# Optimization experiments

Measured on AMD Instinct MI355X. Metric: run time of the kernel, lower is better.

The kernel has to match this reference:

```python
import jax, jax.numpy as jnp
import numpy as np

ETA = 0.1
DT = 1.0
H, DH = 8, 64


def setup_inputs() -> dict:
    key = jax.random.key(0)
    ks = jax.random.split(key, 7)
    B, N, D = 4, 2048, 1024
    s = 0.02
    return {
        "x": jax.random.normal(ks[0], (B, N, D), dtype=jnp.float32),
        "gamma": jax.random.uniform(ks[1], (B, N), dtype=jnp.float32),
        "state": jnp.zeros((B, H, DH, DH), dtype=jnp.float32),
        "Wq": (jax.random.normal(ks[2], (D, H * DH), dtype=jnp.float32) * s),
        "Wk": (jax.random.normal(ks[3], (D, H * DH), dtype=jnp.float32) * s),
        "Wv": (jax.random.normal(ks[4], (D, H * DH), dtype=jnp.float32) * s),
        "Wo": (jax.random.normal(ks[5], (H * DH, D), dtype=jnp.float32) * s),
        "bo": jnp.zeros((D,), dtype=jnp.float32),
    }


def reference(x, gamma, state, Wq, Wk, Wv, Wo, bo):
    B, N, D = x.shape
    # projections -> (N, B, H, DH) for scan over time
    q = (x @ Wq).reshape(B, N, H, DH).transpose(1, 0, 2, 3)
    k = (x @ Wk).reshape(B, N, H, DH).transpose(1, 0, 2, 3)
    v = (x @ Wv).reshape(B, N, H, DH).transpose(1, 0, 2, 3)
    # decay = exp(-clamp(gamma*dt, max=10)) -> (N, B)
    decay = jnp.exp(-jnp.minimum(gamma * DT, 10.0)).T

    def step(st, inp):
        q_t, k_t, v_t, d_t = inp  # (B,H,DH),(B,H,DH),(B,H,DH),(B,)
        # W_new = exp(-Gamma*dt) * stop_grad(W_old) + eta * k^T v
        st_new = d_t[:, None, None, None] * jax.lax.stop_gradient(st) \
                 + ETA * jnp.einsum('bhi,bhj->bhij', k_t, v_t)
        y_t = jnp.einsum('bhij,bhj->bhi', st_new, q_t)  # (B,H,DH)
        return st_new, y_t

    state_final, ys = jax.lax.scan(step, state, (q, k, v, decay))
    # ys: (N, B, H, DH) -> (B, N, H*DH)
    y = ys.transpose(1, 0, 2, 3).reshape(B, N, H * DH)
    out = y @ Wo + bo
    return out, state_final
```

## Files before the change

kernel.cpp:

```cpp
#include <hip/hip_runtime.h>

#define ETA 0.1f
#define BATCH 4
#define SEQ 2048
#define DMODEL 1024
#define NH 8
#define DHEAD 64
#define HD 512
#define QKVW 1536
#define CH 64
#define NCH (SEQ / CH)

typedef float f32x4 __attribute__((ext_vector_type(4)));
typedef short short8 __attribute__((ext_vector_type(8)));
typedef short short4v __attribute__((ext_vector_type(4)));

static __device__ __forceinline__ ushort f2bf(float f) {
  union { float f; unsigned u; } x; x.f = f;
  unsigned r = (x.u + 0x7fffu + ((x.u >> 16) & 1u)) >> 16;
  return (ushort)r;
}
static __device__ __forceinline__ float bf2f(ushort u) {
  union { unsigned u; float f; } x; x.u = ((unsigned)u) << 16;
  return x.f;
}

#define GLDS16(g, l)                                                    \
  __builtin_amdgcn_global_load_lds(                                     \
      (const __attribute__((address_space(1))) unsigned int*)(const void*)(g), \
      (__attribute__((address_space(3))) unsigned int*)(void*)(l), 16, 0, 0)

__global__ __launch_bounds__(256) void convx_kernel(
    const float* __restrict__ x, ushort* __restrict__ xb) {
  size_t i = ((size_t)blockIdx.x * 256 + threadIdx.x) * 16;
  ushort t[16];
#pragma unroll
  for (int u = 0; u < 4; ++u) {
    f32x4 v = *(const f32x4*)&x[i + u * 4];
#pragma unroll
    for (int e = 0; e < 4; ++e) t[u * 4 + e] = f2bf(v[e]);
  }
  *(short8*)&xb[i] = *(short8*)&t[0];
  *(short8*)&xb[i + 8] = *(short8*)&t[8];
}

__global__ __launch_bounds__(256) void convw_kernel(
    const float* __restrict__ Wq, const float* __restrict__ Wk,
    const float* __restrict__ Wv, const float* __restrict__ Wo,
    ushort* __restrict__ Wt, ushort* __restrict__ Wot) {
  const int m = blockIdx.y;
  const int bx = blockIdx.x;
  const int tid = threadIdx.x;
  __shared__ float T[32][33];

  const float* src;
  ushort* dst;
  int srcN, dstK, k0, n0, rowOff;
  if (m < 3) {
    src = (m == 0) ? Wq : ((m == 1) ? Wk : Wv);
    srcN = 512; dstK = 1024;
    k0 = (bx >> 4) << 5; n0 = (bx & 15) << 5;
    dst = Wt; rowOff = m * 512;
  } else {
    src = Wo; srcN = 1024; dstK = 512;
    k0 = (bx >> 5) << 5; n0 = (bx & 31) << 5;
    dst = Wot; rowOff = 0;
  }
  const int r = tid >> 3, c4 = (tid & 7) << 2;
  f32x4 v = *(const f32x4*)&src[(size_t)(k0 + r) * srcN + n0 + c4];
  T[r][c4 + 0] = v[0]; T[r][c4 + 1] = v[1];
  T[r][c4 + 2] = v[2]; T[r][c4 + 3] = v[3];
  __syncthreads();
  short4v o;
#pragma unroll
  for (int e = 0; e < 4; ++e) o[e] = (short)f2bf(T[c4 + e][r]);
  *(short4v*)&dst[(size_t)(rowOff + n0 + r) * dstK + k0 + c4] = o;
}

template <bool OUT_BF16>
__global__ __launch_bounds__(512, 4) void gemm_bt_kernel(
    const ushort* __restrict__ A, const ushort* __restrict__ Bt,
    void* __restrict__ Cv, const float* __restrict__ bias,
    int M, int N, int K) {
  const int tiles_n = N >> 8;
  const int nwg = gridDim.x;
  const int bid = blockIdx.x;
  const int swz = (bid & 7) * (nwg >> 3) + (bid >> 3);
  const int bm = swz / tiles_n;
  const int bn = swz % tiles_n;
  const int tid = threadIdx.x;
  const int w = tid >> 6, lane = tid & 63;
  const int wr = w >> 2, wc = w & 3;
  const int fr = lane & 15, fq = lane >> 4;

  __shared__ ushort As[2][128][32];
  __shared__ ushort Bs[2][256][32];

  f32x4 acc[4][4];
#pragma unroll
  for (int mi = 0; mi < 4; ++mi)
#pragma unroll
    for (int ni = 0; ni < 4; ++ni) acc[mi][ni] = f32x4{0.f, 0.f, 0.f, 0.f};

  const int sr = tid >> 2;
  const int sc = (tid & 3) << 3;
  const ushort* ga  = A  + (size_t)(bm * 128 + sr) * K + sc;
  const ushort* gb0 = Bt + (size_t)(bn * 256 + sr) * K + sc;
  const ushort* gb1 = Bt + (size_t)(bn * 256 + 128 + sr) * K + sc;

  const int nt = K >> 5;

  {
    ushort* la = &As[0][0][0] + (size_t)tid * 8;
    ushort* lb = &Bs[0][0][0] + (size_t)tid * 8;
    GLDS16(ga, la);
    GLDS16(gb0, lb);
    GLDS16(gb1, lb + 4096);
  }
  asm volatile("s_waitcnt vmcnt(0)" ::: "memory");
  __syncthreads();

  for (int t = 0; t < nt; ++t) {
    if (t + 1 < nt) {
      const int nb = (t + 1) & 1;
      const int kt = (t + 1) << 5;
      ushort* la = &As[nb][0][0] + (size_t)tid * 8;
      ushort* lb = &Bs[nb][0][0] + (size_t)tid * 8;
      GLDS16(ga + kt, la);
      GLDS16(gb0 + kt, lb);
      GLDS16(gb1 + kt, lb + 4096);
    }
    const int cb = t & 1;
    short8 a[4], b[4];
#pragma unroll
    for (int mi = 0; mi < 4; ++mi)
      a[mi] = *(const short8*)&As[cb][wr * 64 + mi * 16 + fr][fq * 8];
#pragma unroll
    for (int ni = 0; ni < 4; ++ni)
      b[ni] = *(const short8*)&Bs[cb][wc * 64 + ni * 16 + fr][fq * 8];
#pragma unroll
    for (int mi = 0; mi < 4; ++mi)
#pragma unroll
      for (int ni = 0; ni < 4; ++ni)
        acc[mi][ni] = __builtin_amdgcn_mfma_f32_16x16x32_bf16(
            a[mi], b[ni], acc[mi][ni], 0, 0, 0);
    asm volatile("s_waitcnt vmcnt(0)" ::: "memory");
    __syncthreads();
  }

#pragma unroll
  for (int ni = 0; ni < 4; ++ni) {
    const int gc = bn * 256 + wc * 64 + ni * 16 + fr;
    float badd = (!OUT_BF16 && bias) ? bias[gc] : 0.f;
#pragma unroll
    for (int mi = 0; mi < 4; ++mi) {
#pragma unroll
      for (int r = 0; r < 4; ++r) {
        const int gr = bm * 128 + wr * 64 + mi * 16 + fq * 4 + r;
        if (OUT_BF16) {
          ((ushort*)Cv)[(size_t)gr * N + gc] = f2bf(acc[mi][ni][r]);
        } else {
          ((float*)Cv)[(size_t)gr * N + gc] = acc[mi][ni][r] + badd;
        }
      }
    }
  }
}

__global__ __launch_bounds__(256) void intra_kernel(
    const ushort* __restrict__ qkv, const float* __restrict__ gamma,
    ushort* __restrict__ ybf, ushort* __restrict__ S, float* __restrict__ clb) {
  const int bx = blockIdx.x;
  const int c = bx & (NCH - 1);
  const int h = (bx >> 5) & (NH - 1);
  const int b = bx >> 8;
  const int tid = threadIdx.x;
  const int w = tid >> 6, lane = tid & 63;
  const int fr = lane & 15, fq = lane >> 4;

  __shared__ ushort Qs[64][72];
  __shared__ ushort Vs[64][72];
  __shared__ ushort KT[64][72];
  __shared__ ushort VT[64][72];
  __shared__ ushort Ps[64][72];
  __shared__ float cumS[64];
  __shared__ float clS;

  const int p = tid >> 2, d0 = (tid & 3) * 16;
  const ushort* base = &qkv[((size_t)b * SEQ + c * CH + p) * QKVW + h * 64 + d0];
  short8 q0 = *(const short8*)base;
  short8 q1 = *(const short8*)(base + 8);
  short8 k0 = *(const short8*)(base + 512);
  short8 k1 = *(const short8*)(base + 520);
  short8 v0 = *(const short8*)(base + 1024);
  short8 v1 = *(const short8*)(base + 1032);

  if (tid < 64) {
    float g = gamma[(size_t)b * SEQ + c * CH + tid];
    float prod = expf(-fminf(g, 10.f));
#pragma unroll
    for (int off = 1; off < 64; off <<= 1) {
      float o = __shfl_up(prod, off);
      if (tid >= off) prod *= o;
    }
    cumS[tid] = prod;
    if (tid == 63) clS = prod;
  }
  __syncthreads();

  {
    const float cp = cumS[p];
    const float rc = 1.f / cp;
    ushort tq[16], tv[16];
#pragma unroll
    for (int j = 0; j < 8; ++j) {
      tq[j]     = f2bf(bf2f((ushort)q0[j]) * cp);
      tq[8 + j] = f2bf(bf2f((ushort)q1[j]) * cp);
      tv[j]     = f2bf(bf2f((ushort)v0[j]) * rc);
      tv[8 + j] = f2bf(bf2f((ushort)v1[j]) * rc);
      KT[d0 + j][p] = (ushort)k0[j];
      KT[d0 + 8 + j][p] = (ushort)k1[j];
      VT[d0 + j][p] = tv[j];
      VT[d0 + 8 + j][p] = tv[8 + j];
    }
    *(short8*)&Qs[p][d0] = *(short8*)&tq[0];
    *(short8*)&Qs[p][d0 + 8] = *(short8*)&tq[8];
    *(short8*)&Vs[p][d0] = *(short8*)&tv[0];
    *(short8*)&Vs[p][d0 + 8] = *(short8*)&tv[8];
  }
  __syncthreads();

  const int arow = w * 16 + fr;
  {
    short8 a0 = *(const short8*)&Qs[arow][fq * 8];
    short8 a1 = *(const short8*)&Qs[arow][32 + fq * 8];
#pragma unroll
    for (int cf = 0; cf < 4; ++cf) {
      f32x4 acc = {0.f, 0.f, 0.f, 0.f};
      if (cf <= w) {
        short8 b0 = *(const short8*)&Vs[cf * 16 + fr][fq * 8];
        short8 b1 = *(const short8*)&Vs[cf * 16 + fr][32 + fq * 8];
        acc = __builtin_amdgcn_mfma_f32_16x16x32_bf16(a0, b0, acc, 0, 0, 0);
        acc = __builtin_amdgcn_mfma_f32_16x16x32_bf16(a1, b1, acc, 0, 0, 0);
      }
#pragma unroll
      for (int r = 0; r < 4; ++r) {
        int pi = w * 16 + fq * 4 + r, si = cf * 16 + fr;
        Ps[pi][si] = f2bf((si <= pi) ? acc[r] * ETA : 0.f);
      }
    }
  }
  __syncthreads();

  {
    short8 p0 = *(const short8*)&Ps[arow][fq * 8];
    short8 p1 = *(const short8*)&Ps[arow][32 + fq * 8];
    short8 ka0 = *(const short8*)&KT[arow][fq * 8];
    short8 ka1 = *(const short8*)&KT[arow][32 + fq * 8];
    const float scl = ETA * clS;
    const size_t yrow0 = (size_t)b * SEQ + c * CH;
    ushort* Sp = &S[(((size_t)(b * NH + h)) * NCH + c) << 12];
#pragma unroll
    for (int cf = 0; cf < 4; ++cf) {
      short8 bk0 = *(const short8*)&KT[cf * 16 + fr][fq * 8];
      short8 bk1 = *(const short8*)&KT[cf * 16 + fr][32 + fq * 8];
      f32x4 accY = {0.f, 0.f, 0.f, 0.f};
      accY = __builtin_amdgcn_mfma_f32_16x16x32_bf16(p0, bk0, accY, 0, 0, 0);
      accY = __builtin_amdgcn_mfma_f32_16x16x32_bf16(p1, bk1, accY, 0, 0, 0);
      short8 bv0 = *(const short8*)&VT[cf * 16 + fr][fq * 8];
      short8 bv1 = *(const short8*)&VT[cf * 16 + fr][32 + fq * 8];
      f32x4 accS = {0.f, 0.f, 0.f, 0.f};
      accS = __builtin_amdgcn_mfma_f32_16x16x32_bf16(ka0, bv0, accS, 0, 0, 0);
      accS = __builtin_amdgcn_mfma_f32_16x16x32_bf16(ka1, bv1, accS, 0, 0, 0);
#pragma unroll
      for (int r = 0; r < 4; ++r) {
        int row = w * 16 + fq * 4 + r;
        int col = cf * 16 + fr;
        ybf[(yrow0 + row) * HD + h * 64 + col] = f2bf(accY[r]);
        Sp[row * 64 + col] = f2bf(accS[r] * scl);
      }
    }
  }
  if (tid == 0 && h == 0) clb[b * NCH + c] = clS;
}

__global__ __launch_bounds__(256) void prop_kernel(
    const float* __restrict__ state0, const ushort* __restrict__ S,
    const float* __restrict__ clb, ushort* __restrict__ stash,
    float* __restrict__ state_out) {
  const int bh = blockIdx.x >> 2, rg = blockIdx.x & 3;
  const int b = bh >> 3;
  const int tid = threadIdx.x;
  const int i = rg * 16 + (tid >> 4);
  const int j0 = (tid & 15) * 4;
  const size_t off = ((size_t)bh * 64 + i) * 64 + j0;
  const size_t coff = (size_t)i * 64 + j0;

  f32x4 st = *(const f32x4*)&state0[off];
#pragma unroll 4
  for (int c = 0; c < NCH; ++c) {
    const size_t base = (((size_t)bh * NCH + c) << 12) + coff;
    short4v sv;
#pragma unroll
    for (int e = 0; e < 4; ++e) sv[e] = (short)f2bf(st[e]);
    *(short4v*)&stash[base] = sv;
    short4v s = *(const short4v*)&S[base];
    float clv = clb[b * NCH + c];
#pragma unroll
    for (int e = 0; e < 4; ++e) st[e] = st[e] * clv + bf2f((ushort)s[e]);
  }
  *(f32x4*)&state_out[off] = st;
}

__global__ __launch_bounds__(256) void inter_kernel(
    const ushort* __restrict__ qkv, const float* __restrict__ gamma,
    const ushort* __restrict__ stash, ushort* __restrict__ ybf) {
  const int bx = blockIdx.x;
  const int c = bx & (NCH - 1);
  const int h = (bx >> 5) & (NH - 1);
  const int b = bx >> 8;
  const int tid = threadIdx.x;
  const int w = tid >> 6, lane = tid & 63;
  const int fr = lane & 15, fq = lane >> 4;

  __shared__ ushort Qs[64][72];
  __shared__ ushort Bs[64][72];
  __shared__ float cumS[64];

  const int p = tid >> 2, d0 = (tid & 3) * 16;
  const ushort* qp = &qkv[((size_t)b * SEQ + c * CH + p) * QKVW + h * 64 + d0];
  short8 q0 = *(const short8*)qp;
  short8 q1 = *(const short8*)(qp + 8);
  const size_t sb = ((((size_t)(b * NH + h)) * NCH + c) << 12) + (size_t)p * 64 + d0;
  short8 s0 = *(const short8*)&stash[sb];
  short8 s1 = *(const short8*)&stash[sb + 8];

  if (tid < 64) {
    float g = gamma[(size_t)b * SEQ + c * CH + tid];
    float prod = expf(-fminf(g, 10.f));
#pragma unroll
    for (int off = 1; off < 64; off <<= 1) {
      float o = __shfl_up(prod, off);
      if (tid >= off) prod *= o;
    }
    cumS[tid] = prod;
  }
  __syncthreads();

  {
    const float cp = cumS[p];
    ushort tq[16];
#pragma unroll
    for (int j = 0; j < 8; ++j) {
      tq[j]     = f2bf(bf2f((ushort)q0[j]) * cp);
      tq[8 + j] = f2bf(bf2f((ushort)q1[j]) * cp);
    }
    *(short8*)&Qs[p][d0] = *(short8*)&tq[0];
    *(short8*)&Qs[p][d0 + 8] = *(short8*)&tq[8];
    *(short8*)&Bs[p][d0] = s0;
    *(short8*)&Bs[p][d0 + 8] = s1;
  }
  __syncthreads();

  const int arow = w * 16 + fr;
  short8 a0 = *(const short8*)&Qs[arow][fq * 8];
  short8 a1 = *(const short8*)&Qs[arow][32 + fq * 8];
  const size_t yrow0 = (size_t)b * SEQ + c * CH;
#pragma unroll
  for (int cf = 0; cf < 4; ++cf) {
    short8 b0 = *(const short8*)&Bs[cf * 16 + fr][fq * 8];
    short8 b1 = *(const short8*)&Bs[cf * 16 + fr][32 + fq * 8];
    f32x4 acc = {0.f, 0.f, 0.f, 0.f};
    acc = __builtin_amdgcn_mfma_f32_16x16x32_bf16(a0, b0, acc, 0, 0, 0);
    acc = __builtin_amdgcn_mfma_f32_16x16x32_bf16(a1, b1, acc, 0, 0, 0);
#pragma unroll
    for (int r = 0; r < 4; ++r) {
      int row = w * 16 + fq * 4 + r;
      int col = cf * 16 + fr;
      size_t idx = (yrow0 + row) * HD + h * 64 + col;
      ybf[idx] = f2bf(bf2f(ybf[idx]) + acc[r]);
    }
  }
}

extern "C" void kernel_launch(void* const* d_in, const int* in_sizes, int n_in,
                              void* d_out, int out_size, void* d_ws, size_t ws_size,
                              hipStream_t stream) {
  const float* x      = (const float*)d_in[0];
  const float* gamma  = (const float*)d_in[1];
  const float* state0 = (const float*)d_in[2];
  const float* Wq     = (const float*)d_in[3];
  const float* Wk     = (const float*)d_in[4];
  const float* Wv     = (const float*)d_in[5];
  const float* Wo     = (const float*)d_in[6];
  const float* bo     = (const float*)d_in[7];

  float* out = (float*)d_out;
  float* state_out = out + (size_t)BATCH * SEQ * DMODEL;

  const int M = BATCH * SEQ;

  ushort* xb  = (ushort*)d_ws;
  ushort* wt  = xb + (size_t)M * DMODEL;
  ushort* wot = wt + (size_t)QKVW * DMODEL;
  ushort* qkv = wot + (size_t)DMODEL * HD;
  ushort* ybf = qkv + (size_t)M * QKVW;
  ushort* Sb  = ybf + (size_t)M * HD;
  ushort* stash = Sb + (size_t)BATCH * NH * NCH * 4096;
  float*  clb   = (float*)(stash + (size_t)BATCH * NH * NCH * 4096);

  dim3 blk(256);
  dim3 blkg(512);

  convx_kernel<<<dim3((M * DMODEL) / (256 * 16)), blk, 0, stream>>>(x, xb);
  convw_kernel<<<dim3(512, 4), blk, 0, stream>>>(Wq, Wk, Wv, Wo, wt, wot);

  gemm_bt_kernel<true><<<dim3((M / 128) * (QKVW / 256)), blkg, 0, stream>>>(
      xb, wt, qkv, nullptr, M, QKVW, DMODEL);

  intra_kernel<<<dim3(BATCH * NH * NCH), blk, 0, stream>>>(
      qkv, gamma, ybf, Sb, clb);
  prop_kernel<<<dim3(BATCH * NH * 4), blk, 0, stream>>>(
      state0, Sb, clb, stash, state_out);
  inter_kernel<<<dim3(BATCH * NH * NCH), blk, 0, stream>>>(
      qkv, gamma, stash, ybf);

  gemm_bt_kernel<false><<<dim3((M / 128) * (DMODEL / 256)), blkg, 0, stream>>>(
      ybf, wot, out, bo, M, DMODEL, HD);
}
```

Measured before the change: 99.15 us.

## Use 128x128 GEMM tiles with triple-buffered LDS prefetch pipeline

The bf16 GEMM moves from 512-thread 128x256 tiles to 256-thread 128x128 tiles, doubling the block count. It replaces the double buffer with a three-stage LDS ring, issuing loads two tiles ahead. Partial vmcnt waits let later loads stay in flight while the current tile computes. The aim is to hide global-load latency and improve SM fill, at the cost of more B-tile reloads and more blocks.

```diff
diff --git a/kernel.cpp b/kernel.cpp
--- a/kernel.cpp
+++ b/kernel.cpp
@@ -78,11 +78,11 @@
 }
 
 template <bool OUT_BF16>
-__global__ __launch_bounds__(512, 4) void gemm_bt_kernel(
+__global__ __launch_bounds__(256, 3) void gemm_bt_kernel(
     const ushort* __restrict__ A, const ushort* __restrict__ Bt,
     void* __restrict__ Cv, const float* __restrict__ bias,
     int M, int N, int K) {
-  const int tiles_n = N >> 8;
+  const int tiles_n = N >> 7;
   const int nwg = gridDim.x;
   const int bid = blockIdx.x;
   const int swz = (bid & 7) * (nwg >> 3) + (bid >> 3);
@@ -90,11 +90,11 @@
   const int bn = swz % tiles_n;
   const int tid = threadIdx.x;
   const int w = tid >> 6, lane = tid & 63;
-  const int wr = w >> 2, wc = w & 3;
+  const int wr = w >> 1, wc = w & 1;
   const int fr = lane & 15, fq = lane >> 4;
 
-  __shared__ ushort As[2][128][32];
-  __shared__ ushort Bs[2][256][32];
+  __shared__ ushort As[3][128][32];
+  __shared__ ushort Bs[3][128][32];
 
   f32x4 acc[4][4];
 #pragma unroll
@@ -102,35 +102,33 @@
 #pragma unroll
     for (int ni = 0; ni < 4; ++ni) acc[mi][ni] = f32x4{0.f, 0.f, 0.f, 0.f};
 
-  const int sr = tid >> 2;
-  const int sc = (tid & 3) << 3;
-  const ushort* ga  = A  + (size_t)(bm * 128 + sr) * K + sc;
-  const ushort* gb0 = Bt + (size_t)(bn * 256 + sr) * K + sc;
-  const ushort* gb1 = Bt + (size_t)(bn * 256 + 128 + sr) * K + sc;
+  const int lw = lane >> 2;
+  const int lc = (lane & 3) << 3;
+  const ushort* ga = A + (size_t)(bm * 128 + w * 32 + lw) * K + lc;
+  const ushort* gb = Bt + (size_t)(bn * 128 + w * 32 + lw) * K + lc;
+  const size_t rstep = (size_t)16 * K;
 
   const int nt = K >> 5;
 
-  {
-    ushort* la = &As[0][0][0] + (size_t)tid * 8;
-    ushort* lb = &Bs[0][0][0] + (size_t)tid * 8;
-    GLDS16(ga, la);
-    GLDS16(gb0, lb);
-    GLDS16(gb1, lb + 4096);
-  }
-  asm volatile("s_waitcnt vmcnt(0)" ::: "memory");
-  __syncthreads();
+#pragma unroll
+  for (int pt = 0; pt < 3; ++pt) {
+    ushort* la = &As[pt][w * 32][0];
+    ushort* lb = &Bs[pt][w * 32][0];
+    GLDS16(ga + pt * 32, la);
+    GLDS16(ga + pt * 32 + rstep, la + 512);
+    GLDS16(gb + pt * 32, lb);
+    GLDS16(gb + pt * 32 + rstep, lb + 512);
+  }
 
   for (int t = 0; t < nt; ++t) {
-    if (t + 1 < nt) {
-      const int nb = (t + 1) & 1;
-      const int kt = (t + 1) << 5;
-      ushort* la = &As[nb][0][0] + (size_t)tid * 8;
-      ushort* lb = &Bs[nb][0][0] + (size_t)tid * 8;
-      GLDS16(ga + kt, la);
-      GLDS16(gb0 + kt, lb);
-      GLDS16(gb1 + kt, lb + 4096);
-    }
-    const int cb = t & 1;
+    if (t < nt - 2) {
+      asm volatile("s_waitcnt vmcnt(8)\n\ts_barrier" ::: "memory");
+    } else if (t == nt - 2) {
+      asm volatile("s_waitcnt vmcnt(4)\n\ts_barrier" ::: "memory");
+    } else {
+      asm volatile("s_waitcnt vmcnt(0)\n\ts_barrier" ::: "memory");
+    }
+    const int cb = t % 3;
     short8 a[4], b[4];
 #pragma unroll
     for (int mi = 0; mi < 4; ++mi)
@@ -144,13 +142,21 @@
       for (int ni = 0; ni < 4; ++ni)
         acc[mi][ni] = __builtin_amdgcn_mfma_f32_16x16x32_bf16(
             a[mi], b[ni], acc[mi][ni], 0, 0, 0);
-    asm volatile("s_waitcnt vmcnt(0)" ::: "memory");
-    __syncthreads();
+    asm volatile("s_waitcnt lgkmcnt(0)\n\ts_barrier" ::: "memory");
+    if (t + 3 < nt) {
+      const int kt = (t + 3) << 5;
+      ushort* la = &As[cb][w * 32][0];
+      ushort* lb = &Bs[cb][w * 32][0];
+      GLDS16(ga + kt, la);
+      GLDS16(ga + kt + rstep, la + 512);
+      GLDS16(gb + kt, lb);
+      GLDS16(gb + kt + rstep, lb + 512);
+    }
   }
 
 #pragma unroll
   for (int ni = 0; ni < 4; ++ni) {
-    const int gc = bn * 256 + wc * 64 + ni * 16 + fr;
+    const int gc = bn * 128 + wc * 64 + ni * 16 + fr;
     float badd = (!OUT_BF16 && bias) ? bias[gc] : 0.f;
 #pragma unroll
     for (int mi = 0; mi < 4; ++mi) {
@@ -410,12 +416,11 @@
   float*  clb   = (float*)(stash + (size_t)BATCH * NH * NCH * 4096);
 
   dim3 blk(256);
-  dim3 blkg(512);
 
   convx_kernel<<<dim3((M * DMODEL) / (256 * 16)), blk, 0, stream>>>(x, xb);
   convw_kernel<<<dim3(512, 4), blk, 0, stream>>>(Wq, Wk, Wv, Wo, wt, wot);
 
-  gemm_bt_kernel<true><<<dim3((M / 128) * (QKVW / 256)), blkg, 0, stream>>>(
+  gemm_bt_kernel<true><<<dim3((M / 128) * (QKVW / 128)), blk, 0, stream>>>(
       xb, wt, qkv, nullptr, M, QKVW, DMODEL);
 
   intra_kernel<<<dim3(BATCH * NH * NCH), blk, 0, stream>>>(
@@ -425,6 +430,6 @@
   inter_kernel<<<dim3(BATCH * NH * NCH), blk, 0, stream>>>(
       qkv, gamma, stash, ybf);
 
-  gemm_bt_kernel<false><<<dim3((M / 128) * (DMODEL / 256)), blkg, 0, stream>>>(
+  gemm_bt_kernel<false><<<dim3((M / 128) * (DMODEL / 128)), blk, 0, stream>>>(
       ybf, wot, out, bo, M, DMODEL, HD);
 }
```

Measured after the change: 96.05 us. 3.1% less time.
